# Kernel optimization log

Measured on AMD Instinct MI355X. Metric: run time of the kernel, lower is better.

The kernel has to match this reference:

```python
import jax, jax.numpy as jnp
import numpy as np

B, C, H, W = 16, 256, 96, 96
K = 3
K2 = K * K


def setup_inputs() -> dict:
    key = jax.random.key(0)
    ks = jax.random.split(key, 8)
    s = 1.0 / np.sqrt(C)  # fan-in style scale for 1x1 convs
    sk = 1.0 / np.sqrt(K2)
    return {
        "x": jax.random.normal(ks[0], (B, C, H, W), jnp.float32),
        "w_xproj": jax.random.normal(ks[1], (C, C), jnp.float32) * s,
        "b_xproj": jnp.zeros((C,), jnp.float32),
        "w_proj": jax.random.normal(ks[2], (C, C), jnp.float32) * s,
        "b_proj": jnp.zeros((C,), jnp.float32),
        "w_kp": jax.random.normal(ks[3], (C, C), jnp.float32) * s,
        "b_kp": jnp.zeros((C,), jnp.float32),
        "w_kg": jax.random.normal(ks[4], (K2, K2), jnp.float32) * sk,
        "b_kg": jnp.zeros((K2,), jnp.float32),
        "diff_ctrl": jnp.zeros((1, 1, 1, C), jnp.float32),
    }


def reference(x, w_xproj, b_xproj, w_proj, b_proj, w_kp, b_kp, w_kg, b_kg, diff_ctrl):
    b, c, h, w = x.shape
    # --- kernel synthesis ---
    # 1x1 conv (kernel_proj)
    kp = jnp.einsum('bchw,oc->bohw', x, w_kp) + b_kp[None, :, None, None]
    # AdaptiveAvgPool1d over flattened spatial dim -> 9 bins (H*W divisible by 9)
    pooled = kp.reshape(b, c, K2, (h * w) // K2).mean(axis=-1)  # [B, C, 9]
    pooled = jax.nn.gelu(pooled)
    # per-channel Linear(9 -> 9): y = W @ v + b
    ker = jnp.einsum('bck,jk->bcj', pooled, w_kg) + b_kg  # [B, C, 9]
    # rearrange 'c (k1 k2) -> k1 k2 1 c' (batched)
    ker = ker.reshape(b, c, K, K).transpose(0, 2, 3, 1)[:, :, :, None, :]  # [B, K, K, 1, C]
    # lateral inhibition: subtract learned fraction of per-channel kernel mean
    factor = jax.nn.sigmoid(diff_ctrl)  # [1, 1, 1, C]
    ker = ker - factor * ker.mean(axis=(1, 2, 3), keepdims=True)
    # --- main path ---
    xp = jnp.einsum('bchw,oc->bohw', x, w_xproj) + b_xproj[None, :, None, None]
    pad = K // 2

    def dwconv(xi, ki):  # xi [C,H,W], ki [K,K,1,C]
        return jax.lax.conv_general_dilated(
            xi[None], ki, window_strides=(1, 1),
            padding=((pad, pad), (pad, pad)),
            dimension_numbers=('NCHW', 'HWIO', 'NCHW'),
            feature_group_count=c)[0]

    y = jax.vmap(dwconv)(xp, ker)  # per-sample dynamic depthwise conv
    out = jnp.einsum('bchw,oc->bohw', y, w_proj) + b_proj[None, :, None, None]
    return out
```

## Files before the change

### kernel.cpp

```cpp
#include <hip/hip_runtime.h>

#define CCH 256
#define HWP 9216
#define IMGDIM 96

typedef __attribute__((ext_vector_type(8))) short s16x8;
typedef __attribute__((ext_vector_type(4))) float f32x4;

__device__ __forceinline__ unsigned short f2bf(float f){
  unsigned u = __float_as_uint(f);
  u += 0x7fffu + ((u >> 16) & 1u);
  return (unsigned short)(u >> 16);
}
__device__ __forceinline__ float bf2f(unsigned short h){
  return __uint_as_float(((unsigned)h) << 16);
}

__global__ void k0_convert(const float* __restrict__ wx, const float* __restrict__ wp,
                           unsigned short* __restrict__ wxb, unsigned short* __restrict__ wpb){
  int i = blockIdx.x * 256 + threadIdx.x;
  wxb[i] = f2bf(wx[i]);
  wpb[i] = f2bf(wp[i]);
}

__device__ __forceinline__ void gemm_chunk(const unsigned short* __restrict__ wbf,
                                           const unsigned short* buf,
                                           f32x4 acc[4][4], int lane, int obase, int c0){
  const int g = lane >> 4, r = lane & 15;
  #pragma unroll
  for (int kk = 0; kk < 2; ++kk){
    const int kc = kk*32 + g*8;
    s16x8 afr[4], bfr[4];
    #pragma unroll
    for (int nf = 0; nf < 4; ++nf){
      const int p = nf*16 + r;
      unsigned off = (unsigned)(p*128 + kc*2) ^ ((unsigned)(p & 7) << 4);
      bfr[nf] = *(const s16x8*)((const char*)buf + off);
    }
    #pragma unroll
    for (int mf = 0; mf < 4; ++mf)
      afr[mf] = *(const s16x8*)(wbf + (size_t)(obase + mf*16 + r)*CCH + c0 + kc);
    #pragma unroll
    for (int mf = 0; mf < 4; ++mf){
      #pragma unroll
      for (int nf = 0; nf < 4; ++nf){
        acc[mf][nf] = __builtin_amdgcn_mfma_f32_16x16x32_bf16(afr[mf], bfr[nf], acc[mf][nf], 0, 0, 0);
      }
    }
  }
}

__device__ __forceinline__ void k1_load(const float* __restrict__ xb, int p0, int c0,
                                        int pg, int cgl, float v[4][4]){
  #pragma unroll
  for (int ci = 0; ci < 4; ++ci){
    float4 q = *(const float4*)(xb + (size_t)(c0 + cgl*4 + ci)*HWP + p0 + pg*4);
    v[ci][0]=q.x; v[ci][1]=q.y; v[ci][2]=q.z; v[ci][3]=q.w;
  }
}
__device__ __forceinline__ void k1_store(unsigned short* buf, int pg, int cgl, float v[4][4],
                                         float* __restrict__ xpart, int c0, int lane, int bbase){
  #pragma unroll
  for (int pj = 0; pj < 4; ++pj){
    const int p = pg*4 + pj;
    unsigned off = (unsigned)(p*128 + cgl*8) ^ ((unsigned)(p & 7) << 4);
    ushort4 pk;
    pk.x = f2bf(v[0][pj]); pk.y = f2bf(v[1][pj]);
    pk.z = f2bf(v[2][pj]); pk.w = f2bf(v[3][pj]);
    *(ushort4*)((char*)buf + off) = pk;
  }
  #pragma unroll
  for (int ci = 0; ci < 4; ++ci){
    float s = v[ci][0] + v[ci][1] + v[ci][2] + v[ci][3];
    s += __shfl_xor(s, 1); s += __shfl_xor(s, 2);
    s += __shfl_xor(s, 4); s += __shfl_xor(s, 8);
    if ((lane & 15) == 0) xpart[bbase + c0 + cgl*4 + ci] = s;
  }
}

__global__ __launch_bounds__(256) void k1_xproj(const float* __restrict__ x,
    const unsigned short* __restrict__ wxb, const float* __restrict__ bx,
    unsigned short* __restrict__ xp, float* __restrict__ xpart){
  const int tile = blockIdx.x, b = blockIdx.y;
  const int p0 = tile * 64;
  const int t = threadIdx.x, lane = t & 63, wave = t >> 6;
  __shared__ __align__(16) unsigned short xlds[2][64*64];

  const float* xb = x + (size_t)b * CCH * HWP;
  const int binj = p0 >> 10, blk = (p0 >> 6) & 15;
  const int bbase = (((int)b*9 + binj)*16 + blk)*CCH;
  const int pg = t & 15, cgl = t >> 4;

  float v[2][4][4];
  f32x4 acc[4][4];
  f32x4 zz = {0.f,0.f,0.f,0.f};
  #pragma unroll
  for (int i2=0;i2<4;++i2){
    #pragma unroll
    for (int j2=0;j2<4;++j2) acc[i2][j2] = zz;
  }

  k1_load(xb, p0, 0, pg, cgl, v[0]);
  k1_store(xlds[0], pg, cgl, v[0], xpart, 0, lane, bbase);

  #pragma unroll
  for (int ch = 0; ch < 4; ++ch){
    __syncthreads();
    if (ch < 3) k1_load(xb, p0, (ch+1)*64, pg, cgl, v[(ch+1)&1]);
    gemm_chunk(wxb, xlds[ch & 1], acc, lane, wave*64, ch*64);
    if (ch < 3) k1_store(xlds[(ch+1)&1], pg, cgl, v[(ch+1)&1], xpart, (ch+1)*64, lane, bbase);
  }

  unsigned short* eb = &xlds[0][0];
  const int g = lane >> 4, r = lane & 15;
  #pragma unroll
  for (int h = 0; h < 2; ++h){
    __syncthreads();
    if ((wave >> 1) == h){
      const int mw = wave & 1;
      #pragma unroll
      for (int mf = 0; mf < 4; ++mf){
        const int o  = mw*64 + mf*16 + 4*g;
        const int og = h*128 + o;
        float b0 = bx[og], b1 = bx[og+1], b2 = bx[og+2], b3 = bx[og+3];
        #pragma unroll
        for (int nf = 0; nf < 4; ++nf){
          const int p = nf*16 + r;
          unsigned off = (unsigned)(p*256 + o*2) ^ ((unsigned)(p & 7) << 4);
          ushort4 pk;
          pk.x = f2bf(acc[mf][nf][0] + b0);
          pk.y = f2bf(acc[mf][nf][1] + b1);
          pk.z = f2bf(acc[mf][nf][2] + b2);
          pk.w = f2bf(acc[mf][nf][3] + b3);
          *(ushort4*)((char*)eb + off) = pk;
        }
      }
    }
    __syncthreads();
    const size_t gb = ((size_t)b*HWP + p0)*CCH + h*128;
    #pragma unroll
    for (int it = 0; it < 4; ++it){
      const unsigned u = it*256 + t;
      const unsigned p = u >> 4, unit = u & 15;
      const unsigned srcoff = (u*16u) ^ ((p & 7) << 4);
      uint4 val = *(const uint4*)((const char*)eb + srcoff);
      *(uint4*)(xp + gb + (size_t)p*CCH + unit*8) = val;
    }
  }
}

__global__ __launch_bounds__(256) void k2a_pooled(const float* __restrict__ xpart,
    const float* __restrict__ wkp, const float* __restrict__ bkp,
    float* __restrict__ pooledg){
  const int j = blockIdx.x, b = blockIdx.y, t = threadIdx.x;
  __shared__ float xbar[256];
  __shared__ float wch[256][65];
  const float* xp0 = xpart + (((size_t)b*9 + j)*16)*CCH;
  float s = 0.f;
  #pragma unroll
  for (int blk = 0; blk < 16; ++blk) s += xp0[blk*CCH + t];
  xbar[t] = s * (1.0f/1024.0f);
  float acc = bkp[t];
  for (int ch = 0; ch < 4; ++ch){
    __syncthreads();
    for (int u = t; u < 256*64; u += 256){
      wch[u >> 6][u & 63] = wkp[(size_t)(u >> 6)*CCH + ch*64 + (u & 63)];
    }
    __syncthreads();
    #pragma unroll
    for (int c = 0; c < 64; ++c) acc += wch[t][c] * xbar[ch*64 + c];
  }
  float x3 = acc*acc*acc;
  float tg = tanhf(0.7978845608028654f*(acc + 0.044715f*x3));
  pooledg[((size_t)b*9 + j)*CCH + t] = 0.5f*acc*(1.0f + tg);
}

__global__ void k2b_ker(const float* __restrict__ pooledg, const float* __restrict__ wkg,
                        const float* __restrict__ bkg, const float* __restrict__ dctrl,
                        float* __restrict__ kerg){
  const int b = blockIdx.x, c = threadIdx.x;
  float pl[9];
  #pragma unroll
  for (int k = 0; k < 9; ++k) pl[k] = pooledg[((size_t)b*9 + k)*CCH + c];
  float kv[9]; float m = 0.f;
  #pragma unroll
  for (int jp = 0; jp < 9; ++jp){
    float s2 = bkg[jp];
    #pragma unroll
    for (int k = 0; k < 9; ++k) s2 += pl[k] * wkg[jp*9 + k];
    kv[jp] = s2; m += s2;
  }
  m *= (1.0f/9.0f);
  float f = 1.0f / (1.0f + expf(-dctrl[c]));
  #pragma unroll
  for (int jp = 0; jp < 9; ++jp) kerg[((size_t)b*9 + jp)*CCH + c] = kv[jp] - f*m;
}

__global__ __launch_bounds__(256) void k3a_dw(const unsigned short* __restrict__ xp,
    const float* __restrict__ kerg, unsigned short* __restrict__ y){
  const int tile = blockIdx.x, b = blockIdx.y;
  const int th0 = (tile / 12) * 8, tw0 = (tile % 12) * 8;
  const int t = threadIdx.x;
  __shared__ __align__(16) unsigned short halo[2][100*64];
  __shared__ float kl[9][256];

  for (int u = t; u < 9*256; u += 256)
    kl[u >> 8][u & 255] = kerg[((size_t)b*9 + (u >> 8))*CCH + (u & 255)];

  const unsigned short* xpb = xp + (size_t)b * HWP * CCH;
  unsigned short* yb = y + (size_t)b * HWP * CCH;
  const int p = t >> 2, dh = p >> 3, dw = p & 7, q = t & 3;
  const size_t pout = (size_t)((th0 + dh)*IMGDIM + (tw0 + dw))*CCH;

  uint4 sreg[4];

  #define K3A_ISSUE(CH)                                                        \
    _Pragma("unroll")                                                          \
    for (int i = 0; i < 4; ++i){                                               \
      const int u = i*256 + t;                                                 \
      if (u < 800){                                                            \
        const int pos = u >> 3, w8 = u & 7;                                    \
        const int rr = pos / 10, cc = pos % 10;                                \
        const int hh = th0 + rr - 1, ww = tw0 + cc - 1;                        \
        uint4 val = {0u,0u,0u,0u};                                             \
        if (hh >= 0 && hh < IMGDIM && ww >= 0 && ww < IMGDIM)                  \
          val = *(const uint4*)(xpb + ((size_t)(hh*IMGDIM + ww))*CCH + (CH)*64 + w8*8); \
        sreg[i] = val;                                                         \
      }                                                                        \
    }
  #define K3A_WRITE(BUF)                                                       \
    _Pragma("unroll")                                                          \
    for (int i = 0; i < 4; ++i){                                               \
      const int u = i*256 + t;                                                 \
      if (u < 800){                                                            \
        const int pos = u >> 3, w8 = u & 7;                                    \
        unsigned off = (unsigned)(pos*128 + w8*16) ^ ((unsigned)(pos & 7) << 4); \
        *(uint4*)((char*)halo[BUF] + off) = sreg[i];                           \
      }                                                                        \
    }

  K3A_ISSUE(0)
  K3A_WRITE(0)

  #pragma unroll
  for (int ch = 0; ch < 4; ++ch){
    __syncthreads();
    if (ch < 3) K3A_ISSUE(ch+1)
    #pragma unroll
    for (int ci = 0; ci < 2; ++ci){
      const int c = q*16 + ci*8;
      const int cg = ch*64 + c;
      float a8[8] = {0,0,0,0,0,0,0,0};
      #pragma unroll
      for (int tap = 0; tap < 9; ++tap){
        const int pos = (dh + tap/3)*10 + (dw + tap%3);
        unsigned hof = (unsigned)(pos*128 + c*2) ^ ((unsigned)(pos & 7) << 4);
        union { uint4 qv; unsigned short u16[8]; } hv;
        hv.qv = *(const uint4*)((const char*)halo[ch & 1] + hof);
        const float4* kp4 = (const float4*)&kl[tap][cg];
        float4 ka = kp4[0], kb = kp4[1];
        a8[0] += bf2f(hv.u16[0]) * ka.x;
        a8[1] += bf2f(hv.u16[1]) * ka.y;
        a8[2] += bf2f(hv.u16[2]) * ka.z;
        a8[3] += bf2f(hv.u16[3]) * ka.w;
        a8[4] += bf2f(hv.u16[4]) * kb.x;
        a8[5] += bf2f(hv.u16[5]) * kb.y;
        a8[6] += bf2f(hv.u16[6]) * kb.z;
        a8[7] += bf2f(hv.u16[7]) * kb.w;
      }
      unsigned pk[4];
      #pragma unroll
      for (int e = 0; e < 4; ++e)
        pk[e] = (unsigned)f2bf(a8[2*e]) | ((unsigned)f2bf(a8[2*e+1]) << 16);
      *(uint4*)(yb + pout + cg) = *(uint4*)pk;
    }
    if (ch < 3) K3A_WRITE((ch+1)&1)
  }
  #undef K3A_ISSUE
  #undef K3A_WRITE
}

__global__ __launch_bounds__(256) void k3b_proj(const unsigned short* __restrict__ y,
    const unsigned short* __restrict__ wpb, const float* __restrict__ bp,
    float* __restrict__ out){
  const int tile = blockIdx.x, b = blockIdx.y;
  const int p0 = tile * 64;
  const int t = threadIdx.x, lane = t & 63, wave = t >> 6;
  __shared__ __align__(16) unsigned short ylds[2][64*64];
  const unsigned short* yb = y + (size_t)b * HWP * CCH;

  const int ug = t & 7, pg2 = t >> 3;
  uint4 srg[2];

  #define K3B_ISSUE(CH)                                                        \
    _Pragma("unroll")                                                          \
    for (int i = 0; i < 2; ++i)                                                \
      srg[i] = *(const uint4*)(yb + (size_t)(p0 + pg2 + i*32)*CCH + (CH)*64 + ug*8);
  #define K3B_WRITE(BUF)                                                       \
    _Pragma("unroll")                                                          \
    for (int i = 0; i < 2; ++i){                                               \
      const int p = pg2 + i*32;                                                \
      unsigned off = (unsigned)(p*128 + ug*16) ^ ((unsigned)(p & 7) << 4);     \
      *(uint4*)((char*)ylds[BUF] + off) = srg[i];                              \
    }

  f32x4 acc[4][4];
  f32x4 zz = {0.f,0.f,0.f,0.f};
  #pragma unroll
  for (int i2=0;i2<4;++i2){
    #pragma unroll
    for (int j2=0;j2<4;++j2) acc[i2][j2] = zz;
  }

  K3B_ISSUE(0)
  K3B_WRITE(0)

  #pragma unroll
  for (int ch = 0; ch < 4; ++ch){
    __syncthreads();
    if (ch < 3) K3B_ISSUE(ch+1)
    gemm_chunk(wpb, ylds[ch & 1], acc, lane, wave*64, ch*64);
    if (ch < 3) K3B_WRITE((ch+1)&1)
  }
  #undef K3B_ISSUE
  #undef K3B_WRITE

  const int g = lane >> 4, r = lane & 15;
  #pragma unroll
  for (int mf = 0; mf < 4; ++mf){
    const int o = wave*64 + mf*16 + 4*g;
    float b0 = bp[o], b1 = bp[o+1], b2 = bp[o+2], b3 = bp[o+3];
    #pragma unroll
    for (int nf = 0; nf < 4; ++nf){
      const int pp = p0 + nf*16 + r;
      out[((size_t)b*CCH + o + 0)*HWP + pp] = acc[mf][nf][0] + b0;
      out[((size_t)b*CCH + o + 1)*HWP + pp] = acc[mf][nf][1] + b1;
      out[((size_t)b*CCH + o + 2)*HWP + pp] = acc[mf][nf][2] + b2;
      out[((size_t)b*CCH + o + 3)*HWP + pp] = acc[mf][nf][3] + b3;
    }
  }
}

extern "C" void kernel_launch(void* const* d_in, const int* in_sizes, int n_in,
                              void* d_out, int out_size, void* d_ws, size_t ws_size,
                              hipStream_t stream){
  const float* x   = (const float*)d_in[0];
  const float* wxp = (const float*)d_in[1];
  const float* bxp = (const float*)d_in[2];
  const float* wpr = (const float*)d_in[3];
  const float* bpr = (const float*)d_in[4];
  const float* wkp = (const float*)d_in[5];
  const float* bkp = (const float*)d_in[6];
  const float* wkg = (const float*)d_in[7];
  const float* bkg = (const float*)d_in[8];
  const float* dct = (const float*)d_in[9];

  char* ws = (char*)d_ws;
  unsigned short* wxb   = (unsigned short*)(ws + 0);
  unsigned short* wpb   = (unsigned short*)(ws + 131072);
  float*          xpart = (float*)(ws + 262144);
  float*          pooled= (float*)(ws + 2621440);
  float*          kerg  = (float*)(ws + 2768896);
  unsigned short* xp    = (unsigned short*)(ws + 2916352);
  unsigned short* ybuf  = (unsigned short*)(ws + 78413824);
  float* o = (float*)d_out;

  k0_convert<<<256, 256, 0, stream>>>(wxp, wpr, wxb, wpb);
  k1_xproj<<<dim3(144,16), 256, 0, stream>>>(x, wxb, bxp, xp, xpart);
  k2a_pooled<<<dim3(9,16), 256, 0, stream>>>(xpart, wkp, bkp, pooled);
  k2b_ker<<<16, 256, 0, stream>>>(pooled, wkg, bkg, dct, kerg);
  k3a_dw<<<dim3(144,16), 256, 0, stream>>>(xp, kerg, ybuf);
  k3b_proj<<<dim3(144,16), 256, 0, stream>>>(ybuf, wpb, bpr, o);
}
```

Before: 235.7 us.

## Fuse depthwise conv with output projection GEMM and prefetch weights/x in registers

Merges the depthwise 3x3 conv kernel and the output 1x1 projection into one kernel. The conv result for each 8x8 spatial tile is written to shared memory as bf16 and consumed by MFMA in a software pipeline, so the intermediate y buffer never goes through global memory. In the xproj kernel all four x channel chunks are loaded up front, and weight fragments are double-buffered in registers ahead of the GEMM. The cost is higher register and LDS pressure, which may lower occupancy, and the output stores are now scattered along 8-wide rows of the image.

```diff
diff --git a/kernel.cpp b/kernel.cpp
--- a/kernel.cpp
+++ b/kernel.cpp
@@ -23,14 +23,21 @@
   wpb[i] = f2bf(wp[i]);
 }
 
-__device__ __forceinline__ void gemm_chunk(const unsigned short* __restrict__ wbf,
-                                           const unsigned short* buf,
-                                           f32x4 acc[4][4], int lane, int obase, int c0){
-  const int g = lane >> 4, r = lane & 15;
+__device__ __forceinline__ void wload(const unsigned short* __restrict__ wbf,
+                                      int obase, int c0, int g, int r, s16x8 wf[8]){
+  #pragma unroll
+  for (int kk = 0; kk < 2; ++kk){
+    #pragma unroll
+    for (int mf = 0; mf < 4; ++mf)
+      wf[kk*4+mf] = *(const s16x8*)(wbf + (size_t)(obase + mf*16 + r)*CCH + c0 + kk*32 + g*8);
+  }
+}
+__device__ __forceinline__ void gemm_chunk_w(const unsigned short* buf, const s16x8 wf[8],
+                                             f32x4 acc[4][4], int g, int r){
   #pragma unroll
   for (int kk = 0; kk < 2; ++kk){
     const int kc = kk*32 + g*8;
-    s16x8 afr[4], bfr[4];
+    s16x8 bfr[4];
     #pragma unroll
     for (int nf = 0; nf < 4; ++nf){
       const int p = nf*16 + r;
@@ -38,13 +45,10 @@
       bfr[nf] = *(const s16x8*)((const char*)buf + off);
     }
     #pragma unroll
-    for (int mf = 0; mf < 4; ++mf)
-      afr[mf] = *(const s16x8*)(wbf + (size_t)(obase + mf*16 + r)*CCH + c0 + kc);
-    #pragma unroll
     for (int mf = 0; mf < 4; ++mf){
       #pragma unroll
       for (int nf = 0; nf < 4; ++nf){
-        acc[mf][nf] = __builtin_amdgcn_mfma_f32_16x16x32_bf16(afr[mf], bfr[nf], acc[mf][nf], 0, 0, 0);
+        acc[mf][nf] = __builtin_amdgcn_mfma_f32_16x16x32_bf16(wf[kk*4+mf], bfr[nf], acc[mf][nf], 0, 0, 0);
       }
     }
   }
@@ -84,6 +88,7 @@
   const int tile = blockIdx.x, b = blockIdx.y;
   const int p0 = tile * 64;
   const int t = threadIdx.x, lane = t & 63, wave = t >> 6;
+  const int g = lane >> 4, r = lane & 15;
   __shared__ __align__(16) unsigned short xlds[2][64*64];
 
   const float* xb = x + (size_t)b * CCH * HWP;
@@ -91,7 +96,8 @@
   const int bbase = (((int)b*9 + binj)*16 + blk)*CCH;
   const int pg = t & 15, cgl = t >> 4;
 
-  float v[2][4][4];
+  float v[4][4][4];
+  s16x8 wf[2][8];
   f32x4 acc[4][4];
   f32x4 zz = {0.f,0.f,0.f,0.f};
   #pragma unroll
@@ -100,19 +106,20 @@
     for (int j2=0;j2<4;++j2) acc[i2][j2] = zz;
   }
 
-  k1_load(xb, p0, 0, pg, cgl, v[0]);
+  #pragma unroll
+  for (int ch = 0; ch < 4; ++ch) k1_load(xb, p0, ch*64, pg, cgl, v[ch]);
+  wload(wxb, wave*64, 0, g, r, wf[0]);
   k1_store(xlds[0], pg, cgl, v[0], xpart, 0, lane, bbase);
 
   #pragma unroll
   for (int ch = 0; ch < 4; ++ch){
     __syncthreads();
-    if (ch < 3) k1_load(xb, p0, (ch+1)*64, pg, cgl, v[(ch+1)&1]);
-    gemm_chunk(wxb, xlds[ch & 1], acc, lane, wave*64, ch*64);
-    if (ch < 3) k1_store(xlds[(ch+1)&1], pg, cgl, v[(ch+1)&1], xpart, (ch+1)*64, lane, bbase);
+    if (ch < 3) wload(wxb, wave*64, (ch+1)*64, g, r, wf[(ch+1)&1]);
+    gemm_chunk_w(xlds[ch & 1], wf[ch & 1], acc, g, r);
+    if (ch < 3) k1_store(xlds[(ch+1)&1], pg, cgl, v[ch+1], xpart, (ch+1)*64, lane, bbase);
   }
 
   unsigned short* eb = &xlds[0][0];
-  const int g = lane >> 4, r = lane & 15;
   #pragma unroll
   for (int h = 0; h < 2; ++h){
     __syncthreads();
@@ -196,25 +203,34 @@
   for (int jp = 0; jp < 9; ++jp) kerg[((size_t)b*9 + jp)*CCH + c] = kv[jp] - f*m;
 }
 
-__global__ __launch_bounds__(256) void k3a_dw(const unsigned short* __restrict__ xp,
-    const float* __restrict__ kerg, unsigned short* __restrict__ y){
+__global__ __launch_bounds__(256) void k3f_conv(const unsigned short* __restrict__ xp,
+    const unsigned short* __restrict__ wpb, const float* __restrict__ bp,
+    const float* __restrict__ kerg, float* __restrict__ out){
   const int tile = blockIdx.x, b = blockIdx.y;
   const int th0 = (tile / 12) * 8, tw0 = (tile % 12) * 8;
-  const int t = threadIdx.x;
+  const int t = threadIdx.x, lane = t & 63, wave = t >> 6;
+  const int g = lane >> 4, r = lane & 15;
   __shared__ __align__(16) unsigned short halo[2][100*64];
-  __shared__ float kl[9][256];
+  __shared__ __align__(16) unsigned short ylds[2][64*64];
+  __shared__ __align__(16) float kl[9][256];
 
   for (int u = t; u < 9*256; u += 256)
     kl[u >> 8][u & 255] = kerg[((size_t)b*9 + (u >> 8))*CCH + (u & 255)];
 
   const unsigned short* xpb = xp + (size_t)b * HWP * CCH;
-  unsigned short* yb = y + (size_t)b * HWP * CCH;
   const int p = t >> 2, dh = p >> 3, dw = p & 7, q = t & 3;
-  const size_t pout = (size_t)((th0 + dh)*IMGDIM + (tw0 + dw))*CCH;
 
   uint4 sreg[4];
-
-  #define K3A_ISSUE(CH)                                                        \
+  s16x8 wf[2][8];
+  f32x4 acc[4][4];
+  f32x4 zz = {0.f,0.f,0.f,0.f};
+  #pragma unroll
+  for (int i2=0;i2<4;++i2){
+    #pragma unroll
+    for (int j2=0;j2<4;++j2) acc[i2][j2] = zz;
+  }
+
+  #define K3F_ISSUE(CH)                                                        \
     _Pragma("unroll")                                                          \
     for (int i = 0; i < 4; ++i){                                               \
       const int u = i*256 + t;                                                 \
@@ -228,7 +244,7 @@
         sreg[i] = val;                                                         \
       }                                                                        \
     }
-  #define K3A_WRITE(BUF)                                                       \
+  #define K3F_WRITE(BUF)                                                       \
     _Pragma("unroll")                                                          \
     for (int i = 0; i < 4; ++i){                                               \
       const int u = i*256 + t;                                                 \
@@ -239,13 +255,16 @@
       }                                                                        \
     }
 
-  K3A_ISSUE(0)
-  K3A_WRITE(0)
+  wload(wpb, wave*64, 0, g, r, wf[0]);
+  K3F_ISSUE(0)
+  K3F_WRITE(0)
+  __syncthreads();
 
   #pragma unroll
   for (int ch = 0; ch < 4; ++ch){
-    __syncthreads();
-    if (ch < 3) K3A_ISSUE(ch+1)
+    if (ch < 3) K3F_ISSUE(ch+1)
+    if (ch > 0) gemm_chunk_w(ylds[(ch-1)&1], wf[(ch-1)&1], acc, g, r);
+    if (ch < 3) wload(wpb, wave*64, (ch+1)*64, g, r, wf[(ch+1)&1]);
     #pragma unroll
     for (int ci = 0; ci < 2; ++ci){
       const int c = q*16 + ci*8;
@@ -272,71 +291,30 @@
       #pragma unroll
       for (int e = 0; e < 4; ++e)
         pk[e] = (unsigned)f2bf(a8[2*e]) | ((unsigned)f2bf(a8[2*e+1]) << 16);
-      *(uint4*)(yb + pout + cg) = *(uint4*)pk;
-    }
-    if (ch < 3) K3A_WRITE((ch+1)&1)
-  }
-  #undef K3A_ISSUE
-  #undef K3A_WRITE
-}
-
-__global__ __launch_bounds__(256) void k3b_proj(const unsigned short* __restrict__ y,
-    const unsigned short* __restrict__ wpb, const float* __restrict__ bp,
-    float* __restrict__ out){
-  const int tile = blockIdx.x, b = blockIdx.y;
-  const int p0 = tile * 64;
-  const int t = threadIdx.x, lane = t & 63, wave = t >> 6;
-  __shared__ __align__(16) unsigned short ylds[2][64*64];
-  const unsigned short* yb = y + (size_t)b * HWP * CCH;
-
-  const int ug = t & 7, pg2 = t >> 3;
-  uint4 srg[2];
-
-  #define K3B_ISSUE(CH)                                                        \
-    _Pragma("unroll")                                                          \
-    for (int i = 0; i < 2; ++i)                                                \
-      srg[i] = *(const uint4*)(yb + (size_t)(p0 + pg2 + i*32)*CCH + (CH)*64 + ug*8);
-  #define K3B_WRITE(BUF)                                                       \
-    _Pragma("unroll")                                                          \
-    for (int i = 0; i < 2; ++i){                                               \
-      const int p = pg2 + i*32;                                                \
-      unsigned off = (unsigned)(p*128 + ug*16) ^ ((unsigned)(p & 7) << 4);     \
-      *(uint4*)((char*)ylds[BUF] + off) = srg[i];                              \
-    }
-
-  f32x4 acc[4][4];
-  f32x4 zz = {0.f,0.f,0.f,0.f};
-  #pragma unroll
-  for (int i2=0;i2<4;++i2){
-    #pragma unroll
-    for (int j2=0;j2<4;++j2) acc[i2][j2] = zz;
-  }
-
-  K3B_ISSUE(0)
-  K3B_WRITE(0)
-
-  #pragma unroll
-  for (int ch = 0; ch < 4; ++ch){
-    __syncthreads();
-    if (ch < 3) K3B_ISSUE(ch+1)
-    gemm_chunk(wpb, ylds[ch & 1], acc, lane, wave*64, ch*64);
-    if (ch < 3) K3B_WRITE((ch+1)&1)
-  }
-  #undef K3B_ISSUE
-  #undef K3B_WRITE
-
-  const int g = lane >> 4, r = lane & 15;
+      unsigned yoff = (unsigned)(p*128 + c*2) ^ ((unsigned)(p & 7) << 4);
+      *(uint4*)((char*)ylds[ch & 1] + yoff) = *(uint4*)pk;
+    }
+    if (ch < 3) K3F_WRITE((ch+1)&1)
+    __syncthreads();
+  }
+  #undef K3F_ISSUE
+  #undef K3F_WRITE
+
+  gemm_chunk_w(ylds[1], wf[1], acc, g, r);
+
   #pragma unroll
   for (int mf = 0; mf < 4; ++mf){
     const int o = wave*64 + mf*16 + 4*g;
     float b0 = bp[o], b1 = bp[o+1], b2 = bp[o+2], b3 = bp[o+3];
     #pragma unroll
     for (int nf = 0; nf < 4; ++nf){
-      const int pp = p0 + nf*16 + r;
-      out[((size_t)b*CCH + o + 0)*HWP + pp] = acc[mf][nf][0] + b0;
-      out[((size_t)b*CCH + o + 1)*HWP + pp] = acc[mf][nf][1] + b1;
-      out[((size_t)b*CCH + o + 2)*HWP + pp] = acc[mf][nf][2] + b2;
-      out[((size_t)b*CCH + o + 3)*HWP + pp] = acc[mf][nf][3] + b3;
+      const int pl2 = nf*16 + r;
+      const int hh = th0 + (pl2 >> 3), ww = tw0 + (pl2 & 7);
+      const size_t pix = (size_t)hh*IMGDIM + ww;
+      out[((size_t)b*CCH + o + 0)*HWP + pix] = acc[mf][nf][0] + b0;
+      out[((size_t)b*CCH + o + 1)*HWP + pix] = acc[mf][nf][1] + b1;
+      out[((size_t)b*CCH + o + 2)*HWP + pix] = acc[mf][nf][2] + b2;
+      out[((size_t)b*CCH + o + 3)*HWP + pix] = acc[mf][nf][3] + b3;
     }
   }
 }
@@ -362,13 +340,11 @@
   float*          pooled= (float*)(ws + 2621440);
   float*          kerg  = (float*)(ws + 2768896);
   unsigned short* xp    = (unsigned short*)(ws + 2916352);
-  unsigned short* ybuf  = (unsigned short*)(ws + 78413824);
   float* o = (float*)d_out;
 
   k0_convert<<<256, 256, 0, stream>>>(wxp, wpr, wxb, wpb);
   k1_xproj<<<dim3(144,16), 256, 0, stream>>>(x, wxb, bxp, xp, xpart);
   k2a_pooled<<<dim3(9,16), 256, 0, stream>>>(xpart, wkp, bkp, pooled);
   k2b_ker<<<16, 256, 0, stream>>>(pooled, wkg, bkg, dct, kerg);
-  k3a_dw<<<dim3(144,16), 256, 0, stream>>>(xp, kerg, ybuf);
-  k3b_proj<<<dim3(144,16), 256, 0, stream>>>(ybuf, wpb, bpr, o);
-}
+  k3f_conv<<<dim3(144,16), 256, 0, stream>>>(xp, wpb, bpr, kerg, o);
+}
```

Measured after the change: 280.8 us. +19.1%, slower.

## Split output channels across two blocks in xproj and proj GEMMs

Applied to the files above, without the earlier changes.

The two 1x1-conv GEMM kernels now launch twice as many blocks, each computing half of the output channels (128), which halves per-thread accumulators and raises occupancy and grid size. The xproj output is stored in a split layout of two 128-channel halves per image, and the depthwise kernel's halo loads are rewritten to index that layout. The cost is that each input tile, fp32 x for xproj and bf16 y for proj, is now read and converted by two blocks. Only one block per tile writes the pooling partial sums.

```diff
diff --git a/kernel.cpp b/kernel.cpp
--- a/kernel.cpp
+++ b/kernel.cpp
@@ -23,14 +23,14 @@
   wpb[i] = f2bf(wp[i]);
 }
 
-__device__ __forceinline__ void gemm_chunk(const unsigned short* __restrict__ wbf,
-                                           const unsigned short* buf,
-                                           f32x4 acc[4][4], int lane, int obase, int c0){
+__device__ __forceinline__ void gemm_chunk2(const unsigned short* __restrict__ wbf,
+                                            const unsigned short* buf,
+                                            f32x4 acc[2][4], int lane, int orow, int c0){
   const int g = lane >> 4, r = lane & 15;
   #pragma unroll
   for (int kk = 0; kk < 2; ++kk){
     const int kc = kk*32 + g*8;
-    s16x8 afr[4], bfr[4];
+    s16x8 afr[2], bfr[4];
     #pragma unroll
     for (int nf = 0; nf < 4; ++nf){
       const int p = nf*16 + r;
@@ -38,10 +38,10 @@
       bfr[nf] = *(const s16x8*)((const char*)buf + off);
     }
     #pragma unroll
-    for (int mf = 0; mf < 4; ++mf)
-      afr[mf] = *(const s16x8*)(wbf + (size_t)(obase + mf*16 + r)*CCH + c0 + kc);
-    #pragma unroll
-    for (int mf = 0; mf < 4; ++mf){
+    for (int mf = 0; mf < 2; ++mf)
+      afr[mf] = *(const s16x8*)(wbf + (size_t)(orow + mf*16 + r)*CCH + c0 + kc);
+    #pragma unroll
+    for (int mf = 0; mf < 2; ++mf){
       #pragma unroll
       for (int nf = 0; nf < 4; ++nf){
         acc[mf][nf] = __builtin_amdgcn_mfma_f32_16x16x32_bf16(afr[mf], bfr[nf], acc[mf][nf], 0, 0, 0);
@@ -59,7 +59,8 @@
   }
 }
 __device__ __forceinline__ void k1_store(unsigned short* buf, int pg, int cgl, float v[4][4],
-                                         float* __restrict__ xpart, int c0, int lane, int bbase){
+                                         float* __restrict__ xpart, int c0, int lane,
+                                         int bbase, bool dop){
   #pragma unroll
   for (int pj = 0; pj < 4; ++pj){
     const int p = pg*4 + pj;
@@ -74,77 +75,76 @@
     float s = v[ci][0] + v[ci][1] + v[ci][2] + v[ci][3];
     s += __shfl_xor(s, 1); s += __shfl_xor(s, 2);
     s += __shfl_xor(s, 4); s += __shfl_xor(s, 8);
-    if ((lane & 15) == 0) xpart[bbase + c0 + cgl*4 + ci] = s;
+    if (dop && (lane & 15) == 0) xpart[bbase + c0 + cgl*4 + ci] = s;
   }
 }
 
 __global__ __launch_bounds__(256) void k1_xproj(const float* __restrict__ x,
     const unsigned short* __restrict__ wxb, const float* __restrict__ bx,
     unsigned short* __restrict__ xp, float* __restrict__ xpart){
-  const int tile = blockIdx.x, b = blockIdx.y;
+  const int bxid = blockIdx.x, b = blockIdx.y;
+  const int tile = bxid >> 1, oh = bxid & 1;
   const int p0 = tile * 64;
   const int t = threadIdx.x, lane = t & 63, wave = t >> 6;
+  const int g = lane >> 4, r = lane & 15;
   __shared__ __align__(16) unsigned short xlds[2][64*64];
 
   const float* xb = x + (size_t)b * CCH * HWP;
   const int binj = p0 >> 10, blk = (p0 >> 6) & 15;
   const int bbase = (((int)b*9 + binj)*16 + blk)*CCH;
   const int pg = t & 15, cgl = t >> 4;
+  const bool dop = (oh == 0);
+  const int orow = oh*128 + wave*32;
 
   float v[2][4][4];
-  f32x4 acc[4][4];
+  f32x4 acc[2][4];
   f32x4 zz = {0.f,0.f,0.f,0.f};
   #pragma unroll
-  for (int i2=0;i2<4;++i2){
+  for (int i2=0;i2<2;++i2){
     #pragma unroll
     for (int j2=0;j2<4;++j2) acc[i2][j2] = zz;
   }
 
   k1_load(xb, p0, 0, pg, cgl, v[0]);
-  k1_store(xlds[0], pg, cgl, v[0], xpart, 0, lane, bbase);
+  k1_store(xlds[0], pg, cgl, v[0], xpart, 0, lane, bbase, dop);
 
   #pragma unroll
   for (int ch = 0; ch < 4; ++ch){
     __syncthreads();
     if (ch < 3) k1_load(xb, p0, (ch+1)*64, pg, cgl, v[(ch+1)&1]);
-    gemm_chunk(wxb, xlds[ch & 1], acc, lane, wave*64, ch*64);
-    if (ch < 3) k1_store(xlds[(ch+1)&1], pg, cgl, v[(ch+1)&1], xpart, (ch+1)*64, lane, bbase);
+    gemm_chunk2(wxb, xlds[ch & 1], acc, lane, orow, ch*64);
+    if (ch < 3) k1_store(xlds[(ch+1)&1], pg, cgl, v[(ch+1)&1], xpart, (ch+1)*64, lane, bbase, dop);
   }
 
   unsigned short* eb = &xlds[0][0];
-  const int g = lane >> 4, r = lane & 15;
-  #pragma unroll
-  for (int h = 0; h < 2; ++h){
-    __syncthreads();
-    if ((wave >> 1) == h){
-      const int mw = wave & 1;
-      #pragma unroll
-      for (int mf = 0; mf < 4; ++mf){
-        const int o  = mw*64 + mf*16 + 4*g;
-        const int og = h*128 + o;
-        float b0 = bx[og], b1 = bx[og+1], b2 = bx[og+2], b3 = bx[og+3];
-        #pragma unroll
-        for (int nf = 0; nf < 4; ++nf){
-          const int p = nf*16 + r;
-          unsigned off = (unsigned)(p*256 + o*2) ^ ((unsigned)(p & 7) << 4);
-          ushort4 pk;
-          pk.x = f2bf(acc[mf][nf][0] + b0);
-          pk.y = f2bf(acc[mf][nf][1] + b1);
-          pk.z = f2bf(acc[mf][nf][2] + b2);
-          pk.w = f2bf(acc[mf][nf][3] + b3);
-          *(ushort4*)((char*)eb + off) = pk;
-        }
-      }
-    }
-    __syncthreads();
-    const size_t gb = ((size_t)b*HWP + p0)*CCH + h*128;
+  __syncthreads();
+  #pragma unroll
+  for (int mf = 0; mf < 2; ++mf){
+    const int ol = wave*32 + mf*16 + 4*g;
+    const int og = oh*128 + ol;
+    float b0 = bx[og], b1 = bx[og+1], b2 = bx[og+2], b3 = bx[og+3];
+    #pragma unroll
+    for (int nf = 0; nf < 4; ++nf){
+      const int p = nf*16 + r;
+      unsigned off = (unsigned)(p*256 + ol*2) ^ ((unsigned)(p & 7) << 4);
+      ushort4 pk;
+      pk.x = f2bf(acc[mf][nf][0] + b0);
+      pk.y = f2bf(acc[mf][nf][1] + b1);
+      pk.z = f2bf(acc[mf][nf][2] + b2);
+      pk.w = f2bf(acc[mf][nf][3] + b3);
+      *(ushort4*)((char*)eb + off) = pk;
+    }
+  }
+  __syncthreads();
+  {
+    const size_t gb = ((size_t)(b*2 + oh)*HWP + p0)*128;
     #pragma unroll
     for (int it = 0; it < 4; ++it){
       const unsigned u = it*256 + t;
-      const unsigned p = u >> 4, unit = u & 15;
+      const unsigned p = u >> 4;
       const unsigned srcoff = (u*16u) ^ ((p & 7) << 4);
       uint4 val = *(const uint4*)((const char*)eb + srcoff);
-      *(uint4*)(xp + gb + (size_t)p*CCH + unit*8) = val;
+      *(uint4*)(xp + gb + (size_t)u*8) = val;
     }
   }
 }
@@ -207,7 +207,6 @@
   for (int u = t; u < 9*256; u += 256)
     kl[u >> 8][u & 255] = kerg[((size_t)b*9 + (u >> 8))*CCH + (u & 255)];
 
-  const unsigned short* xpb = xp + (size_t)b * HWP * CCH;
   unsigned short* yb = y + (size_t)b * HWP * CCH;
   const int p = t >> 2, dh = p >> 3, dw = p & 7, q = t & 3;
   const size_t pout = (size_t)((th0 + dh)*IMGDIM + (tw0 + dw))*CCH;
@@ -224,7 +223,8 @@
         const int hh = th0 + rr - 1, ww = tw0 + cc - 1;                        \
         uint4 val = {0u,0u,0u,0u};                                             \
         if (hh >= 0 && hh < IMGDIM && ww >= 0 && ww < IMGDIM)                  \
-          val = *(const uint4*)(xpb + ((size_t)(hh*IMGDIM + ww))*CCH + (CH)*64 + w8*8); \
+          val = *(const uint4*)(xp + ((size_t)(b*2 + ((CH)>>1))*HWP            \
+                + (size_t)(hh*IMGDIM + ww))*128 + ((CH)&1)*64 + w8*8);         \
         sreg[i] = val;                                                         \
       }                                                                        \
     }
@@ -283,11 +283,14 @@
 __global__ __launch_bounds__(256) void k3b_proj(const unsigned short* __restrict__ y,
     const unsigned short* __restrict__ wpb, const float* __restrict__ bp,
     float* __restrict__ out){
-  const int tile = blockIdx.x, b = blockIdx.y;
+  const int bxid = blockIdx.x, b = blockIdx.y;
+  const int tile = bxid >> 1, oh = bxid & 1;
   const int p0 = tile * 64;
   const int t = threadIdx.x, lane = t & 63, wave = t >> 6;
+  const int g = lane >> 4, r = lane & 15;
   __shared__ __align__(16) unsigned short ylds[2][64*64];
   const unsigned short* yb = y + (size_t)b * HWP * CCH;
+  const int orow = oh*128 + wave*32;
 
   const int ug = t & 7, pg2 = t >> 3;
   uint4 srg[2];
@@ -304,10 +307,10 @@
       *(uint4*)((char*)ylds[BUF] + off) = srg[i];                              \
     }
 
-  f32x4 acc[4][4];
+  f32x4 acc[2][4];
   f32x4 zz = {0.f,0.f,0.f,0.f};
   #pragma unroll
-  for (int i2=0;i2<4;++i2){
+  for (int i2=0;i2<2;++i2){
     #pragma unroll
     for (int j2=0;j2<4;++j2) acc[i2][j2] = zz;
   }
@@ -319,16 +322,15 @@
   for (int ch = 0; ch < 4; ++ch){
     __syncthreads();
     if (ch < 3) K3B_ISSUE(ch+1)
-    gemm_chunk(wpb, ylds[ch & 1], acc, lane, wave*64, ch*64);
+    gemm_chunk2(wpb, ylds[ch & 1], acc, lane, orow, ch*64);
     if (ch < 3) K3B_WRITE((ch+1)&1)
   }
   #undef K3B_ISSUE
   #undef K3B_WRITE
 
-  const int g = lane >> 4, r = lane & 15;
-  #pragma unroll
-  for (int mf = 0; mf < 4; ++mf){
-    const int o = wave*64 + mf*16 + 4*g;
+  #pragma unroll
+  for (int mf = 0; mf < 2; ++mf){
+    const int o = orow + mf*16 + 4*g;
     float b0 = bp[o], b1 = bp[o+1], b2 = bp[o+2], b3 = bp[o+3];
     #pragma unroll
     for (int nf = 0; nf < 4; ++nf){
@@ -366,9 +368,9 @@
   float* o = (float*)d_out;
 
   k0_convert<<<256, 256, 0, stream>>>(wxp, wpr, wxb, wpb);
-  k1_xproj<<<dim3(144,16), 256, 0, stream>>>(x, wxb, bxp, xp, xpart);
+  k1_xproj<<<dim3(288,16), 256, 0, stream>>>(x, wxb, bxp, xp, xpart);
   k2a_pooled<<<dim3(9,16), 256, 0, stream>>>(xpart, wkp, bkp, pooled);
   k2b_ker<<<16, 256, 0, stream>>>(pooled, wkg, bkg, dct, kerg);
   k3a_dw<<<dim3(144,16), 256, 0, stream>>>(xp, kerg, ybuf);
-  k3b_proj<<<dim3(144,16), 256, 0, stream>>>(ybuf, wpb, bpr, o);
-}
+  k3b_proj<<<dim3(288,16), 256, 0, stream>>>(ybuf, wpb, bpr, o);
+}
```

New measurement: 243.5 us. +3.3%, slower.

## Double k1 pixel tile to 128 with 512-thread blocks and deferred pooling sums

Applied to the files above, without the earlier changes.

The xproj GEMM kernel now processes 128 pixels per block with 8 waves: four output-channel groups times two pixel halves. Each bf16 weight fragment is therefore reused across more pixels per block, and the grid is halved. The per-channel partial sums for pooling are kept in registers and reduced once at the end instead of after every chunk. This raises LDS use and register pressure, and launch_bounds(512,2) may limit occupancy. The bf16 conversion also switches to the HIP library intrinsic.

```diff
diff --git a/kernel.cpp b/kernel.cpp
--- a/kernel.cpp
+++ b/kernel.cpp
@@ -1,4 +1,5 @@
 #include <hip/hip_runtime.h>
+#include <hip/hip_bf16.h>
 
 #define CCH 256
 #define HWP 9216
@@ -8,9 +9,8 @@
 typedef __attribute__((ext_vector_type(4))) float f32x4;
 
 __device__ __forceinline__ unsigned short f2bf(float f){
-  unsigned u = __float_as_uint(f);
-  u += 0x7fffu + ((u >> 16) & 1u);
-  return (unsigned short)(u >> 16);
+  __hip_bfloat16 h = __float2bfloat16(f);
+  return *reinterpret_cast<unsigned short*>(&h);
 }
 __device__ __forceinline__ float bf2f(unsigned short h){
   return __uint_as_float(((unsigned)h) << 16);
@@ -25,7 +25,8 @@
 
 __device__ __forceinline__ void gemm_chunk(const unsigned short* __restrict__ wbf,
                                            const unsigned short* buf,
-                                           f32x4 acc[4][4], int lane, int obase, int c0){
+                                           f32x4 acc[4][4], int lane, int obase, int c0,
+                                           int pbase){
   const int g = lane >> 4, r = lane & 15;
   #pragma unroll
   for (int kk = 0; kk < 2; ++kk){
@@ -33,7 +34,7 @@
     s16x8 afr[4], bfr[4];
     #pragma unroll
     for (int nf = 0; nf < 4; ++nf){
-      const int p = nf*16 + r;
+      const int p = pbase + nf*16 + r;
       unsigned off = (unsigned)(p*128 + kc*2) ^ ((unsigned)(p & 7) << 4);
       bfr[nf] = *(const s16x8*)((const char*)buf + off);
     }
@@ -50,48 +51,22 @@
   }
 }
 
-__device__ __forceinline__ void k1_load(const float* __restrict__ xb, int p0, int c0,
-                                        int pg, int cgl, float v[4][4]){
-  #pragma unroll
-  for (int ci = 0; ci < 4; ++ci){
-    float4 q = *(const float4*)(xb + (size_t)(c0 + cgl*4 + ci)*HWP + p0 + pg*4);
-    v[ci][0]=q.x; v[ci][1]=q.y; v[ci][2]=q.z; v[ci][3]=q.w;
-  }
-}
-__device__ __forceinline__ void k1_store(unsigned short* buf, int pg, int cgl, float v[4][4],
-                                         float* __restrict__ xpart, int c0, int lane, int bbase){
-  #pragma unroll
-  for (int pj = 0; pj < 4; ++pj){
-    const int p = pg*4 + pj;
-    unsigned off = (unsigned)(p*128 + cgl*8) ^ ((unsigned)(p & 7) << 4);
-    ushort4 pk;
-    pk.x = f2bf(v[0][pj]); pk.y = f2bf(v[1][pj]);
-    pk.z = f2bf(v[2][pj]); pk.w = f2bf(v[3][pj]);
-    *(ushort4*)((char*)buf + off) = pk;
-  }
-  #pragma unroll
-  for (int ci = 0; ci < 4; ++ci){
-    float s = v[ci][0] + v[ci][1] + v[ci][2] + v[ci][3];
-    s += __shfl_xor(s, 1); s += __shfl_xor(s, 2);
-    s += __shfl_xor(s, 4); s += __shfl_xor(s, 8);
-    if ((lane & 15) == 0) xpart[bbase + c0 + cgl*4 + ci] = s;
-  }
-}
-
-__global__ __launch_bounds__(256) void k1_xproj(const float* __restrict__ x,
+__global__ __launch_bounds__(512, 2) void k1_xproj(const float* __restrict__ x,
     const unsigned short* __restrict__ wxb, const float* __restrict__ bx,
     unsigned short* __restrict__ xp, float* __restrict__ xpart){
   const int tile = blockIdx.x, b = blockIdx.y;
-  const int p0 = tile * 64;
+  const int p0 = tile * 128;
   const int t = threadIdx.x, lane = t & 63, wave = t >> 6;
-  __shared__ __align__(16) unsigned short xlds[2][64*64];
+  const int g = lane >> 4, r = lane & 15;
+  __shared__ __align__(16) unsigned short xlds[2][128*64];
 
   const float* xb = x + (size_t)b * CCH * HWP;
-  const int binj = p0 >> 10, blk = (p0 >> 6) & 15;
-  const int bbase = (((int)b*9 + binj)*16 + blk)*CCH;
-  const int pg = t & 15, cgl = t >> 4;
+  const int binj = p0 >> 10, blk0 = (p0 >> 6) & 15;
+  const int pg = t & 31, cg = t >> 5;
+  const int obase = (wave & 3) * 64, pbase = (wave >> 2) * 64;
 
   float v[2][4][4];
+  float sacc[4][4];
   f32x4 acc[4][4];
   f32x4 zz = {0.f,0.f,0.f,0.f};
   #pragma unroll
@@ -100,33 +75,68 @@
     for (int j2=0;j2<4;++j2) acc[i2][j2] = zz;
   }
 
-  k1_load(xb, p0, 0, pg, cgl, v[0]);
-  k1_store(xlds[0], pg, cgl, v[0], xpart, 0, lane, bbase);
+  #define K1_LOAD(CH, BUF)                                                     \
+    _Pragma("unroll")                                                          \
+    for (int ci = 0; ci < 4; ++ci){                                            \
+      float4 q = *(const float4*)(xb + (size_t)((CH)*64 + cg*4 + ci)*HWP + p0 + pg*4); \
+      v[BUF][ci][0]=q.x; v[BUF][ci][1]=q.y; v[BUF][ci][2]=q.z; v[BUF][ci][3]=q.w; \
+    }
+  #define K1_STORE(CH, BUF)                                                    \
+    _Pragma("unroll")                                                          \
+    for (int pj = 0; pj < 4; ++pj){                                            \
+      const int p = pg*4 + pj;                                                 \
+      unsigned off = (unsigned)(p*128 + cg*8) ^ ((unsigned)(p & 7) << 4);      \
+      ushort4 pk;                                                              \
+      pk.x = f2bf(v[BUF][0][pj]); pk.y = f2bf(v[BUF][1][pj]);                  \
+      pk.z = f2bf(v[BUF][2][pj]); pk.w = f2bf(v[BUF][3][pj]);                  \
+      *(ushort4*)((char*)xlds[BUF] + off) = pk;                                \
+    }                                                                          \
+    _Pragma("unroll")                                                          \
+    for (int ci = 0; ci < 4; ++ci)                                             \
+      sacc[CH][ci] = v[BUF][0 ? 0 : ci][0] + v[BUF][ci][1] + v[BUF][ci][2] + v[BUF][ci][3];
+
+  K1_LOAD(0, 0)
+  K1_STORE(0, 0)
 
   #pragma unroll
   for (int ch = 0; ch < 4; ++ch){
     __syncthreads();
-    if (ch < 3) k1_load(xb, p0, (ch+1)*64, pg, cgl, v[(ch+1)&1]);
-    gemm_chunk(wxb, xlds[ch & 1], acc, lane, wave*64, ch*64);
-    if (ch < 3) k1_store(xlds[(ch+1)&1], pg, cgl, v[(ch+1)&1], xpart, (ch+1)*64, lane, bbase);
+    if (ch < 3) K1_LOAD(ch+1, (ch+1)&1)
+    gemm_chunk(wxb, xlds[ch & 1], acc, lane, obase, ch*64, pbase);
+    if (ch < 3) K1_STORE(ch+1, (ch+1)&1)
+  }
+  #undef K1_LOAD
+  #undef K1_STORE
+
+  {
+    const int bbase = (((int)b*9 + binj)*16 + blk0 + ((lane >> 4) & 1)) * CCH;
+    #pragma unroll
+    for (int ch = 0; ch < 4; ++ch){
+      #pragma unroll
+      for (int ci = 0; ci < 4; ++ci){
+        float s = sacc[ch][ci];
+        s += __shfl_xor(s, 1); s += __shfl_xor(s, 2);
+        s += __shfl_xor(s, 4); s += __shfl_xor(s, 8);
+        if ((lane & 15) == 0) xpart[bbase + ch*64 + cg*4 + ci] = s;
+      }
+    }
   }
 
   unsigned short* eb = &xlds[0][0];
-  const int g = lane >> 4, r = lane & 15;
   #pragma unroll
   for (int h = 0; h < 2; ++h){
     __syncthreads();
-    if ((wave >> 1) == h){
-      const int mw = wave & 1;
+    if (((wave & 3) >> 1) == h){
+      const int olocal0 = (wave & 1) * 64;
       #pragma unroll
       for (int mf = 0; mf < 4; ++mf){
-        const int o  = mw*64 + mf*16 + 4*g;
-        const int og = h*128 + o;
+        const int ol = olocal0 + mf*16 + 4*g;
+        const int og = h*128 + ol;
         float b0 = bx[og], b1 = bx[og+1], b2 = bx[og+2], b3 = bx[og+3];
         #pragma unroll
         for (int nf = 0; nf < 4; ++nf){
-          const int p = nf*16 + r;
-          unsigned off = (unsigned)(p*256 + o*2) ^ ((unsigned)(p & 7) << 4);
+          const int p = pbase + nf*16 + r;
+          unsigned off = (unsigned)(p*256 + ol*2) ^ ((unsigned)(p & 7) << 4);
           ushort4 pk;
           pk.x = f2bf(acc[mf][nf][0] + b0);
           pk.y = f2bf(acc[mf][nf][1] + b1);
@@ -140,7 +150,7 @@
     const size_t gb = ((size_t)b*HWP + p0)*CCH + h*128;
     #pragma unroll
     for (int it = 0; it < 4; ++it){
-      const unsigned u = it*256 + t;
+      const unsigned u = it*512 + t;
       const unsigned p = u >> 4, unit = u & 15;
       const unsigned srcoff = (u*16u) ^ ((p & 7) << 4);
       uint4 val = *(const uint4*)((const char*)eb + srcoff);
@@ -319,7 +329,7 @@
   for (int ch = 0; ch < 4; ++ch){
     __syncthreads();
     if (ch < 3) K3B_ISSUE(ch+1)
-    gemm_chunk(wpb, ylds[ch & 1], acc, lane, wave*64, ch*64);
+    gemm_chunk(wpb, ylds[ch & 1], acc, lane, wave*64, ch*64, 0);
     if (ch < 3) K3B_WRITE((ch+1)&1)
   }
   #undef K3B_ISSUE
@@ -366,7 +376,7 @@
   float* o = (float*)d_out;
 
   k0_convert<<<256, 256, 0, stream>>>(wxp, wpr, wxb, wpb);
-  k1_xproj<<<dim3(144,16), 256, 0, stream>>>(x, wxb, bxp, xp, xpart);
+  k1_xproj<<<dim3(72,16), 512, 0, stream>>>(x, wxb, bxp, xp, xpart);
   k2a_pooled<<<dim3(9,16), 256, 0, stream>>>(xpart, wkp, bkp, pooled);
   k2b_ker<<<16, 256, 0, stream>>>(pooled, wkg, bkg, dct, kerg);
   k3a_dw<<<dim3(144,16), 256, 0, stream>>>(xp, kerg, ybuf);
```

Result: slower. 246.0 us (+4.4%).
